# Performance work log

Hardware: AMD Instinct MI355X
Metric: run time of the kernel (lower is better)

Reference implementation:

```python
import jax, jax.numpy as jnp
import numpy as np

B, T, H = 128, 2048, 128

def setup_inputs() -> dict:
    key = jax.random.key(0)
    k1, k2, k3, k4, k5, k6 = jax.random.split(key, 6)
    s = 1.0 / np.sqrt(H)
    return {
        "H_pos": jax.random.normal(k1, (B, T, H), jnp.float32),
        "H_dyn": jax.random.normal(k2, (B, T, H), jnp.float32),
        "acc_w": jax.random.uniform(k3, (B, T), jnp.float32),
        "W_h": jax.random.uniform(k4, (H, H), jnp.float32, -s, s),
        "W_d": jax.random.uniform(k5, (H, H), jnp.float32, -s, s),
        "W_a": jax.random.uniform(k6, (H,), jnp.float32, -s, s),
        "b_a": jnp.zeros((), jnp.float32),
        "beta": jnp.zeros((), jnp.float32),
    }

def reference(H_pos, H_dyn, acc_w, W_h, W_d, W_a, b_a, beta):
    # energy: W_a(tanh(W_h H_pos + W_d H_dyn)) -> [B, T]
    z = jnp.tanh(jnp.einsum('bth,oh->bto', H_pos, W_h)
                 + jnp.einsum('bth,oh->bto', H_dyn, W_d))
    energy = jnp.einsum('bth,h->bt', z, W_a) + b_a
    # acceleration normalization
    acc_norm = acc_w / jnp.clip(jnp.max(acc_w, axis=1, keepdims=True), 1e-6)
    beta_pos = jax.nn.softplus(beta)
    alpha = jax.nn.softmax(energy * (1.0 + beta_pos * acc_norm), axis=1)  # [B, T]
    context = jnp.einsum('bt,bth->bh', alpha, H_pos)  # [B, H]
    return (context, alpha)
```

## Files before the change

### kernel.cpp

```cpp
#include <hip/hip_runtime.h>

#define B_ 128
#define T_ 2048
#define H_ 128

typedef __attribute__((ext_vector_type(8))) short short8;
typedef __attribute__((ext_vector_type(4))) float f32x4;

__device__ __forceinline__ unsigned short f2b(float f) {
    unsigned int u = __float_as_uint(f);
    u += 0x7fffu + ((u >> 16) & 1u);
    return (unsigned short)(u >> 16);
}
__device__ __forceinline__ short8 pack8(const float4 x, const float4 y) {
    short8 r;
    r[0] = (short)f2b(x.x); r[1] = (short)f2b(x.y);
    r[2] = (short)f2b(x.z); r[3] = (short)f2b(x.w);
    r[4] = (short)f2b(y.x); r[5] = (short)f2b(y.y);
    r[6] = (short)f2b(y.z); r[7] = (short)f2b(y.w);
    return r;
}
__device__ __forceinline__ float tanh_fast(float x) {
    x = fminf(fmaxf(x, -20.f), 20.f);
    float e = __expf(2.f * x);
    return (e - 1.f) / (e + 1.f);
}

__global__ __launch_bounds__(512) void energy_kernel(
    const float* __restrict__ Hp,
    const float* __restrict__ Hd,
    const float* __restrict__ Wh,
    const float* __restrict__ Wd,
    const float* __restrict__ Wa,
    const float* __restrict__ ba_p,
    float* __restrict__ energy,
    int ntiles)
{
    __shared__ unsigned short Wpack[8 * 8 * 64 * 8];
    __shared__ float Was[H_];

    const int tid = threadIdx.x;

    for (int i = tid; i < (H_ * H_) / 4; i += 512) {
        int o  = i >> 5;
        int c4 = i & 31;
        float4 wh = *(const float4*)&Wh[o * H_ + c4 * 4];
        float4 wd = *(const float4*)&Wd[o * H_ + c4 * 4];
        uint2 ph, pdv;
        ph.x  = (unsigned)f2b(wh.x) | ((unsigned)f2b(wh.y) << 16);
        ph.y  = (unsigned)f2b(wh.z) | ((unsigned)f2b(wh.w) << 16);
        pdv.x = (unsigned)f2b(wd.x) | ((unsigned)f2b(wd.y) << 16);
        pdv.y = (unsigned)f2b(wd.z) | ((unsigned)f2b(wd.w) << 16);
        int nt   = o >> 4;
        int l15  = o & 15;
        int kth  = c4 >> 3;
        int lq   = (c4 >> 1) & 3;
        int half = (c4 & 1) * 4;
        int bh = ((kth * 8 + nt) * 64 + lq * 16 + l15) * 8 + half;
        int bd = (((kth + 4) * 8 + nt) * 64 + lq * 16 + l15) * 8 + half;
        *(uint2*)&Wpack[bh] = ph;
        *(uint2*)&Wpack[bd] = pdv;
    }
    if (tid < H_) Was[tid] = Wa[tid];
    __syncthreads();

    const float ba = ba_p[0];

    const int wave = tid >> 6;
    const int lane = tid & 63;
    const int l15  = lane & 15;
    const int lq   = lane >> 4;

    const unsigned short* wb = Wpack + lane * 8;

    const size_t estep = (size_t)gridDim.x * 128 * H_;

    const int row0 = blockIdx.x * 128 + wave * 16;
    const float* pp = Hp + (size_t)(row0 + l15) * H_ + lq * 8;
    const float* pd = Hd + (size_t)(row0 + l15) * H_ + lq * 8;

    float4 abuf[8];
    #pragma unroll
    for (int c = 0; c < 4; c++) {
        abuf[2 * c]     = *(const float4*)(pp + c * 32);
        abuf[2 * c + 1] = *(const float4*)(pp + c * 32 + 4);
    }

    for (int tile = blockIdx.x; tile < ntiles; tile += gridDim.x) {
        const int row_base = tile * 128 + wave * 16;
        const size_t adv = (tile + (int)gridDim.x < ntiles) ? estep : 0;
        const float* ppn = pp + adv;

        f32x4 acc[8];
        #pragma unroll
        for (int nt = 0; nt < 8; nt++) acc[nt] = (f32x4){0.f, 0.f, 0.f, 0.f};

        #pragma unroll
        for (int kt = 0; kt < 8; kt++) {
            const int sl = kt & 3;
            short8 af = pack8(abuf[2 * sl], abuf[2 * sl + 1]);
            const float* s = (kt < 4) ? (pd + kt * 32) : (ppn + (kt - 4) * 32);
            abuf[2 * sl]     = *(const float4*)s;
            abuf[2 * sl + 1] = *(const float4*)(s + 4);
            #pragma unroll
            for (int nt = 0; nt < 8; nt++) {
                short8 bf = *(const short8*)(wb + kt * 4096 + nt * 512);
                acc[nt] = __builtin_amdgcn_mfma_f32_16x16x32_bf16(af, bf, acc[nt], 0, 0, 0);
            }
            __builtin_amdgcn_sched_barrier(0);
        }
        pp = ppn;
        pd += adv;

        float ep[4] = {0.f, 0.f, 0.f, 0.f};
        #pragma unroll
        for (int nt = 0; nt < 8; nt++) {
            const float wa = Was[nt * 16 + l15];
            #pragma unroll
            for (int r = 0; r < 4; r++) ep[r] += tanh_fast(acc[nt][r]) * wa;
        }
        #pragma unroll
        for (int m = 1; m < 16; m <<= 1) {
            #pragma unroll
            for (int r = 0; r < 4; r++) ep[r] += __shfl_xor(ep[r], m, 64);
        }
        if (l15 == 0) {
            #pragma unroll
            for (int r = 0; r < 4; r++)
                energy[row_base + lq * 4 + r] = ep[r] + ba;
        }
    }
}

__global__ __launch_bounds__(256) void softmax_ctx_kernel(
    const float* __restrict__ Hp,
    const float* __restrict__ accw,
    const float* __restrict__ beta_p,
    const float* __restrict__ energy,
    float* __restrict__ out_alpha,
    float* __restrict__ cpart)
{
    __shared__ float al_s[T_];
    __shared__ float red[8 * H_];
    __shared__ float sred[8];

    const int sl   = blockIdx.x & 7;
    const int b    = blockIdx.x >> 3;
    const int tid  = threadIdx.x;
    const int lane = tid & 63;
    const int wid  = tid >> 6;

    const float beta_pos = log1pf(__expf(beta_p[0]));

    float av[8], ev[8];
    {
        const float* pa = accw + b * T_ + tid * 8;
        const float* pe = energy + b * T_ + tid * 8;
        float4 a0 = *(const float4*)pa, a1 = *(const float4*)(pa + 4);
        float4 e0 = *(const float4*)pe, e1 = *(const float4*)(pe + 4);
        av[0]=a0.x; av[1]=a0.y; av[2]=a0.z; av[3]=a0.w;
        av[4]=a1.x; av[5]=a1.y; av[6]=a1.z; av[7]=a1.w;
        ev[0]=e0.x; ev[1]=e0.y; ev[2]=e0.z; ev[3]=e0.w;
        ev[4]=e1.x; ev[5]=e1.y; ev[6]=e1.z; ev[7]=e1.w;
    }
    float amax = -1e30f;
    #pragma unroll
    for (int i = 0; i < 8; i++) amax = fmaxf(amax, av[i]);
    for (int m = 32; m >= 1; m >>= 1) amax = fmaxf(amax, __shfl_xor(amax, m, 64));
    if (lane == 0) sred[wid] = amax;
    __syncthreads();
    if (tid == 0)
        sred[4] = fmaxf(fmaxf(sred[0], sred[1]), fmaxf(sred[2], sred[3]));
    __syncthreads();
    const float invd = beta_pos / fmaxf(sred[4], 1e-6f);

    float sv[8], smax = -1e30f;
    #pragma unroll
    for (int i = 0; i < 8; i++) {
        sv[i] = ev[i] * (1.f + av[i] * invd);
        smax = fmaxf(smax, sv[i]);
    }
    for (int m = 32; m >= 1; m >>= 1) smax = fmaxf(smax, __shfl_xor(smax, m, 64));
    __syncthreads();
    if (lane == 0) sred[wid] = smax;
    __syncthreads();
    if (tid == 0)
        sred[5] = fmaxf(fmaxf(sred[0], sred[1]), fmaxf(sred[2], sred[3]));
    __syncthreads();
    const float smax_all = sred[5];

    float p[8], psum = 0.f;
    #pragma unroll
    for (int i = 0; i < 8; i++) { p[i] = __expf(sv[i] - smax_all); psum += p[i]; }
    for (int m = 32; m >= 1; m >>= 1) psum += __shfl_xor(psum, m, 64);
    __syncthreads();
    if (lane == 0) sred[wid] = psum;
    __syncthreads();
    if (tid == 0)
        sred[6] = sred[0] + sred[1] + sred[2] + sred[3];
    __syncthreads();
    const float invS = 1.f / sred[6];

    #pragma unroll
    for (int i = 0; i < 8; i++) al_s[tid * 8 + i] = p[i] * invS;
    __syncthreads();

    out_alpha[b * T_ + sl * 256 + tid] = al_s[sl * 256 + tid];

    const int row = tid >> 5;
    const int c4  = tid & 31;

    float c0 = 0.f, c1 = 0.f, c2 = 0.f, c3 = 0.f;
    const float* base = Hp + ((size_t)b * T_ + sl * 256) * H_ + c4 * 4;
    const float* al   = al_s + sl * 256;
    #pragma unroll 4
    for (int it = 0; it < 32; it++) {
        int t = it * 8 + row;
        float a = al[t];
        float4 v = *(const float4*)(base + (size_t)t * H_);
        c0 += a * v.x; c1 += a * v.y; c2 += a * v.z; c3 += a * v.w;
    }
    red[row * H_ + c4 * 4 + 0] = c0;
    red[row * H_ + c4 * 4 + 1] = c1;
    red[row * H_ + c4 * 4 + 2] = c2;
    red[row * H_ + c4 * 4 + 3] = c3;
    __syncthreads();
    if (tid < H_) {
        float s = 0.f;
        #pragma unroll
        for (int g = 0; g < 8; g++) s += red[g * H_ + tid];
        cpart[(b * 8 + sl) * H_ + tid] = s;
    }
}

__global__ __launch_bounds__(256) void ctx_reduce_kernel(
    const float* __restrict__ cpart, float* __restrict__ out_ctx)
{
    int i = blockIdx.x * 256 + threadIdx.x;
    if (i < B_ * H_) {
        int b = i >> 7, h = i & 127;
        float s = 0.f;
        #pragma unroll
        for (int g = 0; g < 8; g++) s += cpart[(b * 8 + g) * H_ + h];
        out_ctx[i] = s;
    }
}

extern "C" void kernel_launch(void* const* d_in, const int* in_sizes, int n_in,
                              void* d_out, int out_size, void* d_ws, size_t ws_size,
                              hipStream_t stream) {
    const float* Hp   = (const float*)d_in[0];
    const float* Hd   = (const float*)d_in[1];
    const float* accw = (const float*)d_in[2];
    const float* Wh   = (const float*)d_in[3];
    const float* Wd   = (const float*)d_in[4];
    const float* Wa   = (const float*)d_in[5];
    const float* ba   = (const float*)d_in[6];
    const float* beta = (const float*)d_in[7];

    float* energy_ws = (float*)d_ws;
    float* cpart_ws  = energy_ws + B_ * T_;

    float* out_ctx   = (float*)d_out;
    float* out_alpha = out_ctx + B_ * H_;

    const int ntiles = (B_ * T_) / 128;
    energy_kernel<<<512, 512, 0, stream>>>(Hp, Hd, Wh, Wd, Wa, ba, energy_ws, ntiles);
    softmax_ctx_kernel<<<B_ * 8, 256, 0, stream>>>(Hp, accw, beta, energy_ws, out_alpha, cpart_ws);
    ctx_reduce_kernel<<<(B_ * H_ + 255) / 256, 256, 0, stream>>>(cpart_ws, out_ctx);
}
```

Baseline: 324.5 us.

## Fuse softmax and context into energy kernel with online-softmax tile partials

Each 128-row energy tile now computes its scaled scores, a local max and sum-exp, and an unnormalized partial context. A small combine kernel merges these flash-style to produce alpha and context, and a separate kernel precomputes the acceleration max. This avoids a second full pass over H_pos (128 MB) in a separate kernel, relying on the tile just read staying in cache. The cost is several extra block barriers per tile inside the MFMA loop, plus a second read of H_pos rows that may still go to L2 or HBM.

```diff
diff --git a/kernel.cpp b/kernel.cpp
--- a/kernel.cpp
+++ b/kernel.cpp
@@ -26,18 +26,44 @@
     return (e - 1.f) / (e + 1.f);
 }
 
+__global__ __launch_bounds__(256) void amax_kernel(
+    const float* __restrict__ accw, float* __restrict__ amax_g)
+{
+    __shared__ float wred[4];
+    const int b = blockIdx.x, tid = threadIdx.x;
+    const float* p = accw + (size_t)b * T_ + tid * 8;
+    float4 a0 = *(const float4*)p, a1 = *(const float4*)(p + 4);
+    float m = fmaxf(fmaxf(fmaxf(a0.x, a0.y), fmaxf(a0.z, a0.w)),
+                    fmaxf(fmaxf(a1.x, a1.y), fmaxf(a1.z, a1.w)));
+    for (int d = 32; d >= 1; d >>= 1) m = fmaxf(m, __shfl_xor(m, d, 64));
+    if ((tid & 63) == 0) wred[tid >> 6] = m;
+    __syncthreads();
+    if (tid == 0)
+        amax_g[b] = fmaxf(fmaxf(wred[0], wred[1]), fmaxf(wred[2], wred[3]));
+}
+
 __global__ __launch_bounds__(512) void energy_kernel(
     const float* __restrict__ Hp,
     const float* __restrict__ Hd,
+    const float* __restrict__ accw,
     const float* __restrict__ Wh,
     const float* __restrict__ Wd,
     const float* __restrict__ Wa,
     const float* __restrict__ ba_p,
-    float* __restrict__ energy,
+    const float* __restrict__ beta_p,
+    const float* __restrict__ amax_g,
+    float* __restrict__ s_g,
+    float* __restrict__ ml_g,
+    float* __restrict__ ctxp_g,
     int ntiles)
 {
     __shared__ unsigned short Wpack[8 * 8 * 64 * 8];
     __shared__ float Was[H_];
+    __shared__ float e_s[128];
+    __shared__ float s_s[128];
+    __shared__ float p_s[128];
+    __shared__ float red[16 * H_];
+    __shared__ float mld[2];
 
     const int tid = threadIdx.x;
 
@@ -52,12 +78,12 @@
         pdv.x = (unsigned)f2b(wd.x) | ((unsigned)f2b(wd.y) << 16);
         pdv.y = (unsigned)f2b(wd.z) | ((unsigned)f2b(wd.w) << 16);
         int nt   = o >> 4;
-        int l15  = o & 15;
+        int l15o = o & 15;
         int kth  = c4 >> 3;
         int lq   = (c4 >> 1) & 3;
         int half = (c4 & 1) * 4;
-        int bh = ((kth * 8 + nt) * 64 + lq * 16 + l15) * 8 + half;
-        int bd = (((kth + 4) * 8 + nt) * 64 + lq * 16 + l15) * 8 + half;
+        int bh = ((kth * 8 + nt) * 64 + lq * 16 + l15o) * 8 + half;
+        int bd = (((kth + 4) * 8 + nt) * 64 + lq * 16 + l15o) * 8 + half;
         *(uint2*)&Wpack[bh] = ph;
         *(uint2*)&Wpack[bd] = pdv;
     }
@@ -65,6 +91,7 @@
     __syncthreads();
 
     const float ba = ba_p[0];
+    const float beta_pos = log1pf(__expf(beta_p[0]));
 
     const int wave = tid >> 6;
     const int lane = tid & 63;
@@ -87,7 +114,10 @@
     }
 
     for (int tile = blockIdx.x; tile < ntiles; tile += gridDim.x) {
-        const int row_base = tile * 128 + wave * 16;
+        __syncthreads();
+
+        const int b  = tile >> 4;
+        const int t0 = (tile & 15) * 128;
         const size_t adv = (tile + (int)gridDim.x < ntiles) ? estep : 0;
         const float* ppn = pp + adv;
 
@@ -127,123 +157,103 @@
         if (l15 == 0) {
             #pragma unroll
             for (int r = 0; r < 4; r++)
-                energy[row_base + lq * 4 + r] = ep[r] + ba;
-        }
-    }
-}
-
-__global__ __launch_bounds__(256) void softmax_ctx_kernel(
-    const float* __restrict__ Hp,
-    const float* __restrict__ accw,
-    const float* __restrict__ beta_p,
-    const float* __restrict__ energy,
-    float* __restrict__ out_alpha,
-    float* __restrict__ cpart)
+                e_s[wave * 16 + lq * 4 + r] = ep[r] + ba;
+        }
+        __syncthreads();
+
+        if (tid < 128) {
+            float a = accw[(size_t)b * T_ + t0 + tid];
+            float invd = beta_pos / fmaxf(amax_g[b], 1e-6f);
+            float s = e_s[tid] * (1.f + a * invd);
+            s_s[tid] = s;
+            s_g[(size_t)b * T_ + t0 + tid] = s;
+        }
+        __syncthreads();
+
+        if (wave == 0) {
+            float m = fmaxf(s_s[lane], s_s[lane + 64]);
+            for (int d = 32; d >= 1; d >>= 1) m = fmaxf(m, __shfl_xor(m, d, 64));
+            if (lane == 0) mld[0] = m;
+        }
+        __syncthreads();
+        const float mt = mld[0];
+        if (tid < 128) p_s[tid] = __expf(s_s[tid] - mt);
+        __syncthreads();
+
+        if (wave == 0) {
+            float l = p_s[lane] + p_s[lane + 64];
+            for (int d = 32; d >= 1; d >>= 1) l += __shfl_xor(l, d, 64);
+            if (lane == 0) {
+                ml_g[(b * 16 + (tile & 15)) * 2 + 0] = mt;
+                ml_g[(b * 16 + (tile & 15)) * 2 + 1] = l;
+            }
+        }
+
+        {
+            const int g  = tid >> 5;
+            const int c4 = tid & 31;
+            const float* base = Hp + ((size_t)b * T_ + t0) * H_ + c4 * 4;
+            float c0 = 0.f, c1 = 0.f, c2 = 0.f, c3 = 0.f;
+            #pragma unroll
+            for (int r = 0; r < 8; r++) {
+                int t = r * 16 + g;
+                float pv = p_s[t];
+                float4 v = *(const float4*)(base + (size_t)t * H_);
+                c0 += pv * v.x; c1 += pv * v.y; c2 += pv * v.z; c3 += pv * v.w;
+            }
+            red[g * H_ + c4 * 4 + 0] = c0;
+            red[g * H_ + c4 * 4 + 1] = c1;
+            red[g * H_ + c4 * 4 + 2] = c2;
+            red[g * H_ + c4 * 4 + 3] = c3;
+        }
+        __syncthreads();
+        if (tid < 128) {
+            float s = 0.f;
+            #pragma unroll
+            for (int g = 0; g < 16; g++) s += red[g * H_ + tid];
+            ctxp_g[((size_t)b * 16 + (tile & 15)) * H_ + tid] = s;
+        }
+    }
+}
+
+__global__ __launch_bounds__(256) void combine_kernel(
+    const float* __restrict__ s_g,
+    const float* __restrict__ ml_g,
+    const float* __restrict__ ctxp_g,
+    float* __restrict__ out_ctx,
+    float* __restrict__ out_alpha)
 {
-    __shared__ float al_s[T_];
-    __shared__ float red[8 * H_];
-    __shared__ float sred[8];
-
-    const int sl   = blockIdx.x & 7;
-    const int b    = blockIdx.x >> 3;
-    const int tid  = threadIdx.x;
-    const int lane = tid & 63;
-    const int wid  = tid >> 6;
-
-    const float beta_pos = log1pf(__expf(beta_p[0]));
-
-    float av[8], ev[8];
-    {
-        const float* pa = accw + b * T_ + tid * 8;
-        const float* pe = energy + b * T_ + tid * 8;
-        float4 a0 = *(const float4*)pa, a1 = *(const float4*)(pa + 4);
-        float4 e0 = *(const float4*)pe, e1 = *(const float4*)(pe + 4);
-        av[0]=a0.x; av[1]=a0.y; av[2]=a0.z; av[3]=a0.w;
-        av[4]=a1.x; av[5]=a1.y; av[6]=a1.z; av[7]=a1.w;
-        ev[0]=e0.x; ev[1]=e0.y; ev[2]=e0.z; ev[3]=e0.w;
-        ev[4]=e1.x; ev[5]=e1.y; ev[6]=e1.z; ev[7]=e1.w;
-    }
-    float amax = -1e30f;
+    __shared__ float ml_s[32];
+    const int b = blockIdx.x, tid = threadIdx.x;
+
+    if (tid < 32) ml_s[tid] = ml_g[b * 32 + tid];
+    __syncthreads();
+
+    float M = -1e30f;
     #pragma unroll
-    for (int i = 0; i < 8; i++) amax = fmaxf(amax, av[i]);
-    for (int m = 32; m >= 1; m >>= 1) amax = fmaxf(amax, __shfl_xor(amax, m, 64));
-    if (lane == 0) sred[wid] = amax;
-    __syncthreads();
-    if (tid == 0)
-        sred[4] = fmaxf(fmaxf(sred[0], sred[1]), fmaxf(sred[2], sred[3]));
-    __syncthreads();
-    const float invd = beta_pos / fmaxf(sred[4], 1e-6f);
-
-    float sv[8], smax = -1e30f;
+    for (int i = 0; i < 16; i++) M = fmaxf(M, ml_s[2 * i]);
+    float L = 0.f;
     #pragma unroll
-    for (int i = 0; i < 8; i++) {
-        sv[i] = ev[i] * (1.f + av[i] * invd);
-        smax = fmaxf(smax, sv[i]);
-    }
-    for (int m = 32; m >= 1; m >>= 1) smax = fmaxf(smax, __shfl_xor(smax, m, 64));
-    __syncthreads();
-    if (lane == 0) sred[wid] = smax;
-    __syncthreads();
-    if (tid == 0)
-        sred[5] = fmaxf(fmaxf(sred[0], sred[1]), fmaxf(sred[2], sred[3]));
-    __syncthreads();
-    const float smax_all = sred[5];
-
-    float p[8], psum = 0.f;
-    #pragma unroll
-    for (int i = 0; i < 8; i++) { p[i] = __expf(sv[i] - smax_all); psum += p[i]; }
-    for (int m = 32; m >= 1; m >>= 1) psum += __shfl_xor(psum, m, 64);
-    __syncthreads();
-    if (lane == 0) sred[wid] = psum;
-    __syncthreads();
-    if (tid == 0)
-        sred[6] = sred[0] + sred[1] + sred[2] + sred[3];
-    __syncthreads();
-    const float invS = 1.f / sred[6];
-
-    #pragma unroll
-    for (int i = 0; i < 8; i++) al_s[tid * 8 + i] = p[i] * invS;
-    __syncthreads();
-
-    out_alpha[b * T_ + sl * 256 + tid] = al_s[sl * 256 + tid];
-
-    const int row = tid >> 5;
-    const int c4  = tid & 31;
-
-    float c0 = 0.f, c1 = 0.f, c2 = 0.f, c3 = 0.f;
-    const float* base = Hp + ((size_t)b * T_ + sl * 256) * H_ + c4 * 4;
-    const float* al   = al_s + sl * 256;
-    #pragma unroll 4
-    for (int it = 0; it < 32; it++) {
-        int t = it * 8 + row;
-        float a = al[t];
-        float4 v = *(const float4*)(base + (size_t)t * H_);
-        c0 += a * v.x; c1 += a * v.y; c2 += a * v.z; c3 += a * v.w;
-    }
-    red[row * H_ + c4 * 4 + 0] = c0;
-    red[row * H_ + c4 * 4 + 1] = c1;
-    red[row * H_ + c4 * 4 + 2] = c2;
-    red[row * H_ + c4 * 4 + 3] = c3;
-    __syncthreads();
-    if (tid < H_) {
+    for (int i = 0; i < 16; i++) L += __expf(ml_s[2 * i] - M) * ml_s[2 * i + 1];
+    const float invL = 1.f / L;
+
+    if (tid < 128) {
         float s = 0.f;
         #pragma unroll
-        for (int g = 0; g < 8; g++) s += red[g * H_ + tid];
-        cpart[(b * 8 + sl) * H_ + tid] = s;
-    }
-}
-
-__global__ __launch_bounds__(256) void ctx_reduce_kernel(
-    const float* __restrict__ cpart, float* __restrict__ out_ctx)
-{
-    int i = blockIdx.x * 256 + threadIdx.x;
-    if (i < B_ * H_) {
-        int b = i >> 7, h = i & 127;
-        float s = 0.f;
-        #pragma unroll
-        for (int g = 0; g < 8; g++) s += cpart[(b * 8 + g) * H_ + h];
-        out_ctx[i] = s;
-    }
+        for (int ti = 0; ti < 16; ti++)
+            s += __expf(ml_s[2 * ti] - M) * ctxp_g[((size_t)b * 16 + ti) * H_ + tid];
+        out_ctx[b * H_ + tid] = s * invL;
+    }
+
+    const float* ps = s_g + (size_t)b * T_ + tid * 8;
+    float* pa = out_alpha + (size_t)b * T_ + tid * 8;
+    float4 s0 = *(const float4*)ps, s1 = *(const float4*)(ps + 4);
+    float4 a0, a1;
+    a0.x = __expf(s0.x - M) * invL; a0.y = __expf(s0.y - M) * invL;
+    a0.z = __expf(s0.z - M) * invL; a0.w = __expf(s0.w - M) * invL;
+    a1.x = __expf(s1.x - M) * invL; a1.y = __expf(s1.y - M) * invL;
+    a1.z = __expf(s1.z - M) * invL; a1.w = __expf(s1.w - M) * invL;
+    *(float4*)pa = a0; *(float4*)(pa + 4) = a1;
 }
 
 extern "C" void kernel_launch(void* const* d_in, const int* in_sizes, int n_in,
@@ -258,14 +268,17 @@
     const float* ba   = (const float*)d_in[6];
     const float* beta = (const float*)d_in[7];
 
-    float* energy_ws = (float*)d_ws;
-    float* cpart_ws  = energy_ws + B_ * T_;
+    float* s_ws    = (float*)d_ws;
+    float* ctxp_ws = s_ws + B_ * T_;
+    float* ml_ws   = ctxp_ws + B_ * 16 * H_;
+    float* amax_ws = ml_ws + B_ * 16 * 2;
 
     float* out_ctx   = (float*)d_out;
     float* out_alpha = out_ctx + B_ * H_;
 
     const int ntiles = (B_ * T_) / 128;
-    energy_kernel<<<512, 512, 0, stream>>>(Hp, Hd, Wh, Wd, Wa, ba, energy_ws, ntiles);
-    softmax_ctx_kernel<<<B_ * 8, 256, 0, stream>>>(Hp, accw, beta, energy_ws, out_alpha, cpart_ws);
-    ctx_reduce_kernel<<<(B_ * H_ + 255) / 256, 256, 0, stream>>>(cpart_ws, out_ctx);
-}
+    amax_kernel<<<B_, 256, 0, stream>>>(accw, amax_ws);
+    energy_kernel<<<512, 512, 0, stream>>>(Hp, Hd, accw, Wh, Wd, Wa, ba, beta,
+                                           amax_ws, s_ws, ml_ws, ctxp_ws, ntiles);
+    combine_kernel<<<B_, 256, 0, stream>>>(s_ws, ml_ws, ctxp_ws, out_ctx, out_alpha);
+}
```

New measurement: 309.2 us. -4.7%, faster.
